# Optimization experiments

Measured on AMD Instinct MI355X. Metric: run time of the kernel, lower is better.

The kernel has to match this reference:

```python
import jax, jax.numpy as jnp
import numpy as np

B, T = 64, 512
OBS, DM, DS, NL = 115, 128, 8, 3
EMB, NA, H1 = 16, 19, 256


def _ln(x, g, b, eps=1e-5):
    m = jnp.mean(x, -1, keepdims=True)
    v = jnp.mean((x - m) ** 2, -1, keepdims=True)
    return (x - m) * jax.lax.rsqrt(v + eps) * g + b


def _s6(x, h, lng, lnb, w_ig, w_dt, b_dt, a_log, w_b, w_c, d_par, w_out):
    # x: [B,T,DM], h: [B,DM,DS]
    xn = _ln(x, lng, lnb)
    xp = xn @ w_ig.T                               # [B,T,2*DM]
    x_in, z = xp[..., :DM], xp[..., DM:]
    dt = jax.nn.softplus(x_in @ w_dt.T + b_dt)     # [B,T,DM]
    A = -jnp.exp(a_log)                            # [DM,DS]
    bt = x_in @ w_b.T                              # [B,T,DS]
    ct = x_in @ w_c.T                              # [B,T,DS]
    dA = jnp.exp(dt[..., None] * A)                # [B,T,DM,DS]
    upd = (dt * x_in)[..., None] * bt[:, :, None, :]  # [B,T,DM,DS]

    def step(hc, inp):
        dA_t, u_t, c_t = inp
        hn = dA_t * hc + u_t                       # [B,DM,DS]
        y = jnp.einsum('bds,bs->bd', hn, c_t)      # [B,DM]
        return hn, y

    h_f, ys = jax.lax.scan(
        step, h,
        (jnp.swapaxes(dA, 0, 1), jnp.swapaxes(upd, 0, 1), jnp.swapaxes(ct, 0, 1)))
    y = jnp.swapaxes(ys, 0, 1)                     # [B,T,DM]
    ssm = y * jax.nn.silu(z) + x_in * d_par
    return x + ssm @ w_out.T, h_f.reshape(h_f.shape[0], -1)


def _forward(prev_actions, obs, h0, enc_w1, enc_b1, enc_g1, enc_bb1, enc_w2, enc_b2,
             enc_g2, enc_bb2, emb, proj_w, proj_b, proj_g, proj_bb,
             m_ln_g, m_ln_b, m_w_ig, m_w_dt, m_b_dt, m_a_log, m_w_b, m_w_c, m_d, m_w_out,
             fn_g, fn_b, pol_w1, pol_b1, pol_g, pol_bb, pol_w2, pol_b2):
    # MLP encoder: Linear -> LN -> SiLU -> Linear -> LN (final norm)
    e = jax.nn.silu(_ln(obs @ enc_w1.T + enc_b1, enc_g1, enc_bb1))
    e = _ln(e @ enc_w2.T + enc_b2, enc_g2, enc_bb2)
    pa = emb[prev_actions]                         # [B,T,EMB]
    x = jnp.concatenate([e, pa], -1) @ proj_w.T + proj_b
    x = jax.nn.silu(_ln(x, proj_g, proj_bb))
    for i in range(NL):
        x, _ = _s6(x, h0[i].reshape(-1, DM, DS), m_ln_g[i], m_ln_b[i], m_w_ig[i],
                   m_w_dt[i], m_b_dt[i], m_a_log[i], m_w_b[i], m_w_c[i], m_d[i], m_w_out[i])
    x = _ln(x, fn_g, fn_b)
    p = jax.nn.silu(_ln(x @ pol_w1.T + pol_b1, pol_g, pol_bb))
    return p @ pol_w2.T + pol_b2                   # [B,T,NA] policy logits


def setup_inputs() -> dict:
    key = jax.random.key(0)
    ks = iter(jax.random.split(key, 64))
    def n(shape, s=0.05):
        return jax.random.normal(next(ks), shape, dtype=jnp.float32) * s
    return {
        'obs': jax.random.normal(next(ks), (B, T, OBS), dtype=jnp.float32),
        'h0': jnp.zeros((NL, B, DM * DS), jnp.float32),
        'enc_w1': n((H1, OBS)), 'enc_b1': jnp.zeros((H1,)),
        'enc_g1': jnp.ones((H1,)), 'enc_bb1': jnp.zeros((H1,)),
        'enc_w2': n((DM, H1)), 'enc_b2': jnp.zeros((DM,)),
        'enc_g2': jnp.ones((DM,)), 'enc_bb2': jnp.zeros((DM,)),
        'emb': n((NA + 1, EMB), 1.0),
        'proj_w': n((DM, DM + EMB)), 'proj_b': jnp.zeros((DM,)),
        'proj_g': jnp.ones((DM,)), 'proj_bb': jnp.zeros((DM,)),
        'm_ln_g': jnp.ones((NL, DM)), 'm_ln_b': jnp.zeros((NL, DM)),
        'm_w_ig': n((NL, 2 * DM, DM)), 'm_w_dt': n((NL, DM, DM)),
        'm_b_dt': jnp.zeros((NL, DM)),
        'm_a_log': jax.random.uniform(next(ks), (NL, DM, DS), minval=-3.0, maxval=-1.0, dtype=jnp.float32),
        'm_w_b': n((NL, DS, DM)), 'm_w_c': n((NL, DS, DM)),
        'm_d': jnp.ones((NL, DM)), 'm_w_out': n((NL, DM, DM)),
        'fn_g': jnp.ones((DM,)), 'fn_b': jnp.zeros((DM,)),
        'pol_w1': n((DM, DM)), 'pol_b1': jnp.zeros((DM,)),
        'pol_g': jnp.ones((DM,)), 'pol_bb': jnp.zeros((DM,)),
        'pol_w2': n((NA, DM)), 'pol_b2': jnp.zeros((NA,)),
        'prev_actions': jax.random.randint(next(ks), (B, T), 0, NA + 1),
    }


def reference(obs, h0, enc_w1, enc_b1, enc_g1, enc_bb1, enc_w2, enc_b2, enc_g2, enc_bb2,
              emb, proj_w, proj_b, proj_g, proj_bb, m_ln_g, m_ln_b, m_w_ig, m_w_dt,
              m_b_dt, m_a_log, m_w_b, m_w_c, m_d, m_w_out, fn_g, fn_b, pol_w1, pol_b1,
              pol_g, pol_bb, pol_w2, pol_b2, prev_actions):
    return _forward(prev_actions, obs, h0, enc_w1, enc_b1, enc_g1, enc_bb1, enc_w2,
                    enc_b2, enc_g2, enc_bb2, emb, proj_w, proj_b, proj_g, proj_bb,
                    m_ln_g, m_ln_b, m_w_ig, m_w_dt, m_b_dt, m_a_log, m_w_b, m_w_c,
                    m_d, m_w_out, fn_g, fn_b, pol_w1, pol_b1, pol_g, pol_bb, pol_w2, pol_b2)
```

## Files before the change

kernel.cpp:

```cpp
#include <hip/hip_runtime.h>
#include <math.h>

#define BB 64
#define TT 512
#define OBSD 115
#define DMD 128
#define DSD 8
#define NLD 3
#define EMBD 16
#define NAD 19
#define H1D 256
#define NTOK (BB*TT)
#define SSEG 16
#define TSEG (TT/SSEG)

typedef unsigned short ushort_t;
typedef __attribute__((ext_vector_type(8))) short short8;
typedef __attribute__((ext_vector_type(4))) float f32x4;

__device__ __forceinline__ float silu_f(float x){ return x / (1.f + __expf(-x)); }
__device__ __forceinline__ float softplus_f(float x){
  return fmaxf(x, 0.f) + log1pf(__expf(-fabsf(x)));
}
__device__ __forceinline__ ushort_t f2bf(float x){
  unsigned u = __float_as_uint(x);
  unsigned r = (u + 0x7fffu + ((u >> 16) & 1u)) >> 16;
  return (ushort_t)r;
}
__device__ __forceinline__ float b2f(ushort_t x){
  return __uint_as_float(((unsigned)x) << 16);
}
#define MFMA(a,b,c) __builtin_amdgcn_mfma_f32_16x16x32_bf16((a),(b),(c),0,0,0)
#define LOG2E 1.44269504f

template<int D, int SV>
__device__ __forceinline__ void ln32(const float* s_val, float* s_mr, int tid){
  const int t = tid >> 3, part = tid & 7;
  float s = 0.f, s2 = 0.f;
  #pragma unroll
  for (int j = part; j < D; j += 8){ float v = s_val[t*SV + j]; s += v; s2 = fmaf(v, v, s2); }
  s += __shfl_xor(s, 1, 64); s2 += __shfl_xor(s2, 1, 64);
  s += __shfl_xor(s, 2, 64); s2 += __shfl_xor(s2, 2, 64);
  s += __shfl_xor(s, 4, 64); s2 += __shfl_xor(s2, 4, 64);
  if (part == 0){
    float m = s * (1.f/(float)D);
    s_mr[t*2] = m;
    s_mr[t*2+1] = rsqrtf(s2 * (1.f/(float)D) - m*m + 1e-5f);
  }
}

struct PJob { const float* src; ushort_t* dst; int N; int K; int Kpad; int rowofs; int Nw; };
struct PJobs { PJob j[20]; };

__global__ __launch_bounds__(256) void k_prep(PJobs P){
  const int job = blockIdx.x >> 2;
  const int sub = blockIdx.x & 3;
  PJob pj = P.j[job];
  const int elems = pj.Nw * pj.Kpad;
  for (int idx = sub*256 + threadIdx.x; idx < elems; idx += 4*256){
    int n = idx / pj.Kpad;
    int k = idx - n*pj.Kpad;
    float v = (n < pj.N && k < pj.K) ? pj.src[(size_t)n*pj.K + k] : 0.f;
    pj.dst[(size_t)(pj.rowofs + n)*pj.Kpad + k] = f2bf(v);
  }
}

__global__ __launch_bounds__(256) void k_enc1(
    const float* __restrict__ obs, const ushort_t* __restrict__ w1b,
    const float* __restrict__ b1, const float* __restrict__ g1,
    const float* __restrict__ bb1, ushort_t* __restrict__ e1)
{
  __shared__ ushort_t s_a[32*136];
  __shared__ float s_val[32*264];
  __shared__ float s_mr[64];
  const int tok0 = blockIdx.x * 32;
  const int tid = threadIdx.x;
  const int lane = tid & 63, w = tid >> 6;
  const int q = lane >> 4, cn = lane & 15;
  const int m0 = (w & 1) * 16, nh = w >> 1;

  for (int e = tid; e < 32*16; e += 256){
    int t = e >> 4, kc = e & 15;
    const float* op = obs + (size_t)(tok0 + t)*OBSD;
    short8 v;
    #pragma unroll
    for (int j = 0; j < 8; j++){
      int k = kc*8 + j;
      v[j] = (short)f2bf(k < OBSD ? op[k] : 0.f);
    }
    *(short8*)&s_a[t*136 + kc*8] = v;
  }
  __syncthreads();

  short8 af[4];
  #pragma unroll
  for (int ks = 0; ks < 4; ks++)
    af[ks] = *(const short8*)&s_a[(m0 + cn)*136 + ks*32 + q*8];

  #pragma unroll
  for (int nt = 0; nt < 8; nt++){
    const int n0 = (nh*8 + nt) * 16;
    f32x4 acc = {0.f,0.f,0.f,0.f};
    #pragma unroll
    for (int ks = 0; ks < 4; ks++){
      short8 bf = *(const short8*)&w1b[(size_t)(n0 + cn)*128 + ks*32 + q*8];
      acc = MFMA(af[ks], bf, acc);
    }
    float bias = b1[n0 + cn];
    #pragma unroll
    for (int r = 0; r < 4; r++)
      s_val[(m0 + q*4 + r)*264 + n0 + cn] = acc[r] + bias;
  }
  __syncthreads();

  ln32<256,264>(s_val, s_mr, tid);
  __syncthreads();
  for (int e = tid; e < 32*256; e += 256){
    int t = e >> 8, c = e & 255;
    float v = (s_val[t*264 + c] - s_mr[t*2]) * s_mr[t*2+1] * g1[c] + bb1[c];
    e1[(size_t)(tok0 + t)*256 + c] = f2bf(silu_f(v));
  }
}

__global__ __launch_bounds__(256) void k_enc2p(
    const ushort_t* __restrict__ e1, const ushort_t* __restrict__ w2b,
    const float* __restrict__ b2, const float* __restrict__ g2,
    const float* __restrict__ bb2,
    const float* __restrict__ emb, const int* __restrict__ pact,
    const ushort_t* __restrict__ pwb, const float* __restrict__ pb,
    const float* __restrict__ pg, const float* __restrict__ pbb,
    float* __restrict__ X,
    const float* __restrict__ lng, const float* __restrict__ lnb,
    const ushort_t* __restrict__ wigb, const ushort_t* __restrict__ wdbcb,
    const float* __restrict__ bdt,
    ushort_t* __restrict__ XINb, ushort_t* __restrict__ Zb,
    ushort_t* __restrict__ DTb, ushort_t* __restrict__ BTu, ushort_t* __restrict__ CTu,
    const float* __restrict__ alog0,
    float* __restrict__ HLOC, float* __restrict__ PPR)
{
  __shared__ __align__(16) char sm[46336];
  float*    s_val = (float*)sm;
  ushort_t* s_a   = (ushort_t*)(sm + 17408);
  ushort_t* s_xin = (ushort_t*)(sm + 28160);
  ushort_t* s_dt  = (ushort_t*)(sm + 36864);
  ushort_t* s_btc = (ushort_t*)(sm + 45568);
  float*    s_mr  = (float*)(sm + 46080);

  const int tok0 = blockIdx.x * 32;
  const int bidx = blockIdx.x >> 4;
  const int ch   = blockIdx.x & 15;
  const int tid = threadIdx.x;
  const int lane = tid & 63, w = tid >> 6;
  const int q = lane >> 4, cn = lane & 15;
  const int m0 = (w & 1) * 16, nh = w >> 1;

  for (int e = tid; e < 32*32; e += 256){
    int t = e >> 5, k = e & 31;
    float v = 0.f;
    if (k < EMBD){ int a = pact[tok0 + t]; v = emb[(size_t)a*EMBD + k]; }
    s_a[t*168 + 128 + k] = f2bf(v);
  }
  {
    short8 af[8];
    #pragma unroll
    for (int ks = 0; ks < 8; ks++)
      af[ks] = *(const short8*)&e1[(size_t)(tok0 + m0 + cn)*256 + ks*32 + q*8];
    #pragma unroll
    for (int nt = 0; nt < 4; nt++){
      const int n0 = (nh*4 + nt) * 16;
      f32x4 acc = {0.f,0.f,0.f,0.f};
      #pragma unroll
      for (int ks = 0; ks < 8; ks++){
        short8 bf = *(const short8*)&w2b[(size_t)(n0 + cn)*256 + ks*32 + q*8];
        acc = MFMA(af[ks], bf, acc);
      }
      float bias = b2[n0 + cn];
      #pragma unroll
      for (int r = 0; r < 4; r++)
        s_val[(m0 + q*4 + r)*136 + n0 + cn] = acc[r] + bias;
    }
  }
  __syncthreads();

  ln32<128,136>(s_val, s_mr, tid);
  __syncthreads();
  for (int e = tid; e < 32*128; e += 256){
    int t = e >> 7, c = e & 127;
    float v = (s_val[t*136 + c] - s_mr[t*2]) * s_mr[t*2+1] * g2[c] + bb2[c];
    s_a[t*168 + c] = f2bf(v);
  }
  __syncthreads();

  {
    short8 af2[5];
    #pragma unroll
    for (int ks = 0; ks < 5; ks++)
      af2[ks] = *(const short8*)&s_a[(m0 + cn)*168 + ks*32 + q*8];
    #pragma unroll
    for (int nt = 0; nt < 4; nt++){
      const int n0 = (nh*4 + nt) * 16;
      f32x4 acc = {0.f,0.f,0.f,0.f};
      #pragma unroll
      for (int ks = 0; ks < 5; ks++){
        short8 bf = *(const short8*)&pwb[(size_t)(n0 + cn)*160 + ks*32 + q*8];
        acc = MFMA(af2[ks], bf, acc);
      }
      float bias = pb[n0 + cn];
      #pragma unroll
      for (int r = 0; r < 4; r++)
        s_val[(m0 + q*4 + r)*136 + n0 + cn] = acc[r] + bias;
    }
  }
  __syncthreads();

  ln32<128,136>(s_val, s_mr, tid);
  __syncthreads();
  for (int e = tid; e < 32*128; e += 256){
    int t = e >> 7, c = e & 127;
    float v = (s_val[t*136 + c] - s_mr[t*2]) * s_mr[t*2+1] * pg[c] + pbb[c];
    v = silu_f(v);
    X[(size_t)tok0*128 + e] = v;
    s_val[t*136 + c] = v;
  }
  __syncthreads();

  ln32<128,136>(s_val, s_mr, tid);
  __syncthreads();
  for (int e = tid; e < 32*128; e += 256){
    int t = e >> 7, c = e & 127;
    float v = (s_val[t*136 + c] - s_mr[t*2]) * s_mr[t*2+1] * lng[c] + lnb[c];
    s_a[t*168 + c] = f2bf(v);
  }
  __syncthreads();

  {
    short8 af[4];
    #pragma unroll
    for (int ks = 0; ks < 4; ks++)
      af[ks] = *(const short8*)&s_a[(m0 + cn)*168 + ks*32 + q*8];
    #pragma unroll
    for (int nt = 0; nt < 8; nt++){
      const int n0 = (nh*8 + nt) * 16;
      f32x4 acc = {0.f,0.f,0.f,0.f};
      #pragma unroll
      for (int ks = 0; ks < 4; ks++){
        short8 bf = *(const short8*)&wigb[(size_t)(n0 + cn)*128 + ks*32 + q*8];
        acc = MFMA(af[ks], bf, acc);
      }
      if (n0 < 128){
        #pragma unroll
        for (int r = 0; r < 4; r++){
          int tr = m0 + q*4 + r;
          ushort_t bb = f2bf(acc[r]);
          XINb[(size_t)(tok0 + tr)*128 + n0 + cn] = bb;
          s_xin[tr*136 + n0 + cn] = bb;
        }
      } else {
        #pragma unroll
        for (int r = 0; r < 4; r++){
          int tr = m0 + q*4 + r;
          Zb[(size_t)(tok0 + tr)*128 + (n0 - 128) + cn] = f2bf(acc[r]);
        }
      }
    }
  }
  __syncthreads();

  {
    short8 af2[4];
    #pragma unroll
    for (int ks = 0; ks < 4; ks++)
      af2[ks] = *(const short8*)&s_xin[(m0 + cn)*136 + ks*32 + q*8];
    for (int nt = nh; nt < 9; nt += 2){
      const int n0 = nt * 16;
      f32x4 acc = {0.f,0.f,0.f,0.f};
      #pragma unroll
      for (int ks = 0; ks < 4; ks++){
        short8 bf = *(const short8*)&wdbcb[(size_t)(n0 + cn)*128 + ks*32 + q*8];
        acc = MFMA(af2[ks], bf, acc);
      }
      const int col = n0 + cn;
      if (col < 128){
        float bd = bdt[col];
        #pragma unroll
        for (int r = 0; r < 4; r++){
          int tr = m0 + q*4 + r;
          ushort_t dv = f2bf(softplus_f(acc[r] + bd));
          DTb[(size_t)(tok0 + tr)*128 + col] = dv;
          s_dt[tr*136 + col] = dv;
        }
      } else if (col < 136){
        #pragma unroll
        for (int r = 0; r < 4; r++){
          int tr = m0 + q*4 + r;
          ushort_t bb = f2bf(acc[r]);
          BTu[(size_t)(tok0 + tr)*8 + (col - 128)] = bb;
          s_btc[tr*8 + (col - 128)] = bb;
        }
      } else {
        #pragma unroll
        for (int r = 0; r < 4; r++)
          CTu[(size_t)(tok0 + m0 + q*4 + r)*8 + (col - 136)] = f2bf(acc[r]);
      }
    }
  }
  __syncthreads();

  {
    const int d = tid & 127, sh = tid >> 7;
    float A2c[4], hh[4], pp[4];
    #pragma unroll
    for (int j = 0; j < 4; j++){
      A2c[j] = -__expf(alog0[d*8 + sh*4 + j]) * LOG2E;
      hh[j] = 0.f; pp[j] = 1.f;
    }
    for (int t = 0; t < 32; t++){
      float dt = b2f(s_dt[t*136 + d]);
      float wv = dt * b2f(s_xin[t*136 + d]);
      #pragma unroll
      for (int j = 0; j < 4; j++){
        float dA = exp2f(dt * A2c[j]);
        hh[j] = fmaf(dA, hh[j], wv * b2f(s_btc[t*8 + sh*4 + j]));
        pp[j] *= dA;
      }
    }
    const size_t o = ((size_t)bidx*16 + ch)*1024 + d*8 + sh*4;
    #pragma unroll
    for (int j = 0; j < 4; j++){ HLOC[o+j] = hh[j]; PPR[o+j] = pp[j]; }
  }
}

__global__ __launch_bounds__(256) void k_carry(
    const float* __restrict__ h0g,
    const float* __restrict__ HL, const float* __restrict__ PP,
    float* __restrict__ HST)
{
  const int b = blockIdx.x;
  const int qd = threadIdx.x;
  float4 H = *(const float4*)(h0g + (size_t)b*1024 + qd*4);
  for (int sg = 0; sg < SSEG; sg++){
    *(float4*)(HST + ((size_t)b*SSEG + sg)*1024 + qd*4) = H;
    float4 hl = *(const float4*)(HL + ((size_t)b*SSEG + sg)*1024 + qd*4);
    float4 pp = *(const float4*)(PP + ((size_t)b*SSEG + sg)*1024 + qd*4);
    H.x = fmaf(pp.x, H.x, hl.x); H.y = fmaf(pp.y, H.y, hl.y);
    H.z = fmaf(pp.z, H.z, hl.z); H.w = fmaf(pp.w, H.w, hl.w);
  }
}

#define SMS 34560

__device__ __forceinline__ void phaseB_post(
    const ushort_t* DTb, const ushort_t* XINb, const ushort_t* Zb,
    const ushort_t* BTu, const ushort_t* CTu,
    const float* __restrict__ alog, const float* __restrict__ HST,
    const float* __restrict__ dpar, const ushort_t* __restrict__ woutb,
    float* __restrict__ X, char* sm, int b, int sg)
{
  ushort_t* s_dtS = (ushort_t*)sm;
  ushort_t* s_xiS = (ushort_t*)(sm + 8192);
  ushort_t* s_zS  = (ushort_t*)(sm + 16384);
  ushort_t* s_a   = (ushort_t*)(sm + 24576);
  float*    s_x   = (float*)sm;
  ushort_t* s_bt  = (ushort_t*)(sm + 33280);
  ushort_t* s_ct  = (ushort_t*)(sm + 33792);
  float*    s_mr  = (float*)(sm + 34304);

  const int tid = threadIdx.x;
  const int d = tid;
  const int w = tid >> 6, lane = tid & 63, q = lane >> 4, cn = lane & 15;
  const size_t segtok = (size_t)b*TT + sg*TSEG;

  {
    const uint4* gdt = (const uint4*)(DTb + segtok*128);
    const uint4* gxi = (const uint4*)(XINb + segtok*128);
    const uint4* gz  = (const uint4*)(Zb + segtok*128);
    #pragma unroll
    for (int i = 0; i < 4; i++){
      ((uint4*)s_dtS)[tid + i*128] = gdt[tid + i*128];
      ((uint4*)s_xiS)[tid + i*128] = gxi[tid + i*128];
      ((uint4*)s_zS )[tid + i*128] = gz [tid + i*128];
    }
    ((unsigned*)s_bt)[tid] = ((const unsigned*)(BTu + segtok*8))[tid];
    ((unsigned*)s_ct)[tid] = ((const unsigned*)(CTu + segtok*8))[tid];
  }
  float A2[8], h[8];
  #pragma unroll
  for (int s = 0; s < 8; s++){
    A2[s] = -__expf(alog[d*8 + s]) * LOG2E;
    h[s] = HST[((size_t)b*SSEG + sg)*1024 + d*8 + s];
  }
  const float dp = dpar[d];
  __syncthreads();

  #pragma unroll 4
  for (int t = 0; t < 32; t++){
    float dt = b2f(s_dtS[t*128 + d]);
    float xi = b2f(s_xiS[t*128 + d]);
    float wv = dt * xi;
    float y = 0.f;
    #pragma unroll
    for (int s = 0; s < 8; s++){
      float dA = exp2f(dt * A2[s]);
      h[s] = fmaf(dA, h[s], wv * b2f(s_bt[t*8 + s]));
      y = fmaf(h[s], b2f(s_ct[t*8 + s]), y);
    }
    float ssm = y * silu_f(b2f(s_zS[t*128 + d])) + xi * dp;
    s_a[t*136 + d] = f2bf(ssm);
  }
  __syncthreads();

  {
    short8 af[2][4];
    #pragma unroll
    for (int mt = 0; mt < 2; mt++)
      #pragma unroll
      for (int ks = 0; ks < 4; ks++)
        af[mt][ks] = *(const short8*)&s_a[(mt*16 + cn)*136 + ks*32 + q*8];
    for (int nt = w; nt < 8; nt += 2){
      const int n0 = nt * 16;
      short8 bf[4];
      #pragma unroll
      for (int ks = 0; ks < 4; ks++)
        bf[ks] = *(const short8*)&woutb[(size_t)(n0+cn)*128 + ks*32 + q*8];
      #pragma unroll
      for (int mt = 0; mt < 2; mt++){
        f32x4 acc = {0.f,0.f,0.f,0.f};
        #pragma unroll
        for (int ks = 0; ks < 4; ks++) acc = MFMA(af[mt][ks], bf[ks], acc);
        #pragma unroll
        for (int r = 0; r < 4; r++){
          const int tr = mt*16 + q*4 + r;
          const size_t g = (segtok + tr)*128 + n0 + cn;
          float xn = X[g] + acc[r];
          X[g] = xn;
          s_x[tr*130 + n0 + cn] = xn;
        }
      }
    }
  }
  __syncthreads();

  {
    const int t = tid >> 2, qtr = tid & 3;
    float s = 0.f, s2 = 0.f;
    const float* row = s_x + t*130 + qtr*32;
    for (int j = 0; j < 32; j++){ float v = row[j]; s += v; s2 = fmaf(v, v, s2); }
    s  += __shfl_xor(s, 1, 64);  s2 += __shfl_xor(s2, 1, 64);
    s  += __shfl_xor(s, 2, 64);  s2 += __shfl_xor(s2, 2, 64);
    float m = s * (1.f/128.f);
    float var = s2 * (1.f/128.f) - m*m;
    if (qtr == 0){ s_mr[t*2] = m; s_mr[t*2+1] = rsqrtf(var + 1e-5f); }
  }
  __syncthreads();
}

__global__ __launch_bounds__(128) void k_scan2p(
    ushort_t* DTb, ushort_t* XINb, ushort_t* Zb,
    ushort_t* BTu, ushort_t* CTu,
    const float* __restrict__ alog, const float* __restrict__ HST,
    const float* __restrict__ dpar, const ushort_t* __restrict__ woutb,
    float* __restrict__ X,
    const float* __restrict__ lng, const float* __restrict__ lnb,
    const ushort_t* __restrict__ wigb, const ushort_t* __restrict__ wdbcb,
    const float* __restrict__ bdt,
    const float* __restrict__ alogn,
    float* __restrict__ HLOC, float* __restrict__ PPR)
{
  __shared__ __align__(16) char sm[SMS];
  ushort_t* s_a  = (ushort_t*)(sm + 24576);
  float*    s_x  = (float*)sm;
  ushort_t* s_xin= (ushort_t*)sm;
  ushort_t* s_bt = (ushort_t*)(sm + 33280);
  float*    s_mr = (float*)(sm + 34304);

  const int b = blockIdx.x >> 4, sg = blockIdx.x & 15;
  const int tid = threadIdx.x;
  const int w = tid >> 6, lane = tid & 63, q = lane >> 4, cn = lane & 15;
  const size_t segtok = (size_t)b*TT + sg*TSEG;

  phaseB_post(DTb, XINb, Zb, BTu, CTu, alog, HST, dpar, woutb, X, sm, b, sg);

  {
    float g = lng[tid], c0 = lnb[tid];
    for (int t = 0; t < 32; t++){
      float v = (s_x[t*130 + tid] - s_mr[t*2]) * s_mr[t*2+1] * g + c0;
      s_a[t*136 + tid] = f2bf(v);
    }
  }
  __syncthreads();

  {
    short8 af[2][4];
    #pragma unroll
    for (int mt = 0; mt < 2; mt++)
      #pragma unroll
      for (int ks = 0; ks < 4; ks++)
        af[mt][ks] = *(const short8*)&s_a[(mt*16 + cn)*136 + ks*32 + q*8];
    for (int nt = w; nt < 16; nt += 2){
      const int n0 = nt * 16;
      short8 bf[4];
      #pragma unroll
      for (int ks = 0; ks < 4; ks++)
        bf[ks] = *(const short8*)&wigb[(size_t)(n0+cn)*128 + ks*32 + q*8];
      #pragma unroll
      for (int mt = 0; mt < 2; mt++){
        f32x4 acc = {0.f,0.f,0.f,0.f};
        #pragma unroll
        for (int ks = 0; ks < 4; ks++) acc = MFMA(af[mt][ks], bf[ks], acc);
        if (n0 < 128){
          #pragma unroll
          for (int r = 0; r < 4; r++){
            const int tr = mt*16 + q*4 + r;
            ushort_t bb = f2bf(acc[r]);
            XINb[(segtok + tr)*128 + n0 + cn] = bb;
            s_xin[tr*136 + n0 + cn] = bb;
          }
        } else {
          #pragma unroll
          for (int r = 0; r < 4; r++){
            const int tr = mt*16 + q*4 + r;
            Zb[(segtok + tr)*128 + (n0-128) + cn] = f2bf(acc[r]);
          }
        }
      }
    }
  }
  __syncthreads();

  {
    short8 af[2][4];
    #pragma unroll
    for (int mt = 0; mt < 2; mt++)
      #pragma unroll
      for (int ks = 0; ks < 4; ks++)
        af[mt][ks] = *(const short8*)&s_xin[(mt*16 + cn)*136 + ks*32 + q*8];
    for (int nt = w; nt < 9; nt += 2){
      const int n0 = nt * 16;
      short8 bf[4];
      #pragma unroll
      for (int ks = 0; ks < 4; ks++)
        bf[ks] = *(const short8*)&wdbcb[(size_t)(n0+cn)*128 + ks*32 + q*8];
      const int col = n0 + cn;
      #pragma unroll
      for (int mt = 0; mt < 2; mt++){
        f32x4 acc = {0.f,0.f,0.f,0.f};
        #pragma unroll
        for (int ks = 0; ks < 4; ks++) acc = MFMA(af[mt][ks], bf[ks], acc);
        if (col < 128){
          float bd = bdt[col];
          #pragma unroll
          for (int r = 0; r < 4; r++){
            const int tr = mt*16 + q*4 + r;
            ushort_t dv = f2bf(softplus_f(acc[r] + bd));
            DTb[(segtok + tr)*128 + col] = dv;
            s_a[tr*136 + col] = dv;
          }
        } else if (col < 136){
          #pragma unroll
          for (int r = 0; r < 4; r++){
            const int tr = mt*16 + q*4 + r;
            ushort_t bb = f2bf(acc[r]);
            BTu[(segtok + tr)*8 + (col-128)] = bb;
            s_bt[tr*8 + (col-128)] = bb;
          }
        } else {
          #pragma unroll
          for (int r = 0; r < 4; r++)
            CTu[(segtok + mt*16 + q*4 + r)*8 + (col-136)] = f2bf(acc[r]);
        }
      }
    }
  }
  __syncthreads();

  {
    float A2n[8], hh[8], pp[8];
    #pragma unroll
    for (int s = 0; s < 8; s++){
      A2n[s] = -__expf(alogn[tid*8 + s]) * LOG2E;
      hh[s] = 0.f; pp[s] = 1.f;
    }
    for (int t = 0; t < 32; t++){
      float dt = b2f(s_a[t*136 + tid]);
      float wv = dt * b2f(s_xin[t*136 + tid]);
      #pragma unroll
      for (int s = 0; s < 8; s++){
        float dA = exp2f(dt * A2n[s]);
        hh[s] = fmaf(dA, hh[s], wv * b2f(s_bt[t*8 + s]));
        pp[s] *= dA;
      }
    }
    const size_t o = ((size_t)b*SSEG + sg)*1024 + tid*8;
    #pragma unroll
    for (int s = 0; s < 8; s++){ HLOC[o+s] = hh[s]; PPR[o+s] = pp[s]; }
  }
}

__global__ __launch_bounds__(128) void k_scan2h(
    const ushort_t* DTb, const ushort_t* XINb, const ushort_t* Zb,
    const ushort_t* BTu, const ushort_t* CTu,
    const float* __restrict__ alog, const float* __restrict__ HST,
    const float* __restrict__ dpar, const ushort_t* __restrict__ woutb,
    float* __restrict__ X,
    const float* __restrict__ fng, const float* __restrict__ fnb,
    const ushort_t* __restrict__ pw1b, const float* __restrict__ pb1,
    const float* __restrict__ pg, const float* __restrict__ pbb,
    const ushort_t* __restrict__ pw2b, const float* __restrict__ pb2,
    float* __restrict__ out)
{
  __shared__ __align__(16) char sm[SMS];
  ushort_t* s_a  = (ushort_t*)(sm + 24576);
  float*    s_x  = (float*)sm;
  float*    s_mr = (float*)(sm + 34304);

  const int b = blockIdx.x >> 4, sg = blockIdx.x & 15;
  const int tid = threadIdx.x;
  const int w = tid >> 6, lane = tid & 63, q = lane >> 4, cn = lane & 15;
  const size_t segtok = (size_t)b*TT + sg*TSEG;

  phaseB_post((ushort_t*)DTb, (ushort_t*)XINb, (ushort_t*)Zb,
              (ushort_t*)BTu, (ushort_t*)CTu, alog, HST, dpar, woutb, X, sm, b, sg);

  {
    float g = fng[tid], c0 = fnb[tid];
    for (int t = 0; t < 32; t++){
      float v = (s_x[t*130 + tid] - s_mr[t*2]) * s_mr[t*2+1] * g + c0;
      s_a[t*136 + tid] = f2bf(v);
    }
  }
  __syncthreads();

  {
    short8 af[2][4];
    #pragma unroll
    for (int mt = 0; mt < 2; mt++)
      #pragma unroll
      for (int ks = 0; ks < 4; ks++)
        af[mt][ks] = *(const short8*)&s_a[(mt*16 + cn)*136 + ks*32 + q*8];
    for (int nt = w; nt < 8; nt += 2){
      const int n0 = nt * 16;
      short8 bf[4];
      #pragma unroll
      for (int ks = 0; ks < 4; ks++)
        bf[ks] = *(const short8*)&pw1b[(size_t)(n0+cn)*128 + ks*32 + q*8];
      float bias = pb1[n0 + cn];
      #pragma unroll
      for (int mt = 0; mt < 2; mt++){
        f32x4 acc = {0.f,0.f,0.f,0.f};
        #pragma unroll
        for (int ks = 0; ks < 4; ks++) acc = MFMA(af[mt][ks], bf[ks], acc);
        #pragma unroll
        for (int r = 0; r < 4; r++)
          s_x[(mt*16 + q*4 + r)*130 + n0 + cn] = acc[r] + bias;
      }
    }
  }
  __syncthreads();

  {
    const int t = tid >> 2, qtr = tid & 3;
    float s = 0.f, s2 = 0.f;
    const float* row = s_x + t*130 + qtr*32;
    for (int j = 0; j < 32; j++){ float v = row[j]; s += v; s2 = fmaf(v, v, s2); }
    s  += __shfl_xor(s, 1, 64);  s2 += __shfl_xor(s2, 1, 64);
    s  += __shfl_xor(s, 2, 64);  s2 += __shfl_xor(s2, 2, 64);
    float m = s * (1.f/128.f);
    float var = s2 * (1.f/128.f) - m*m;
    if (qtr == 0){ s_mr[t*2] = m; s_mr[t*2+1] = rsqrtf(var + 1e-5f); }
  }
  __syncthreads();
  {
    float g = pg[tid], c0 = pbb[tid];
    for (int t = 0; t < 32; t++){
      float v = (s_x[t*130 + tid] - s_mr[t*2]) * s_mr[t*2+1] * g + c0;
      s_a[t*136 + tid] = f2bf(silu_f(v));
    }
  }
  __syncthreads();

  {
    short8 af[2][4];
    #pragma unroll
    for (int mt = 0; mt < 2; mt++)
      #pragma unroll
      for (int ks = 0; ks < 4; ks++)
        af[mt][ks] = *(const short8*)&s_a[(mt*16 + cn)*136 + ks*32 + q*8];
    const int n0 = w * 16;
    short8 bf[4];
    #pragma unroll
    for (int ks = 0; ks < 4; ks++)
      bf[ks] = *(const short8*)&pw2b[(size_t)(n0+cn)*128 + ks*32 + q*8];
    const int col = n0 + cn;
    #pragma unroll
    for (int mt = 0; mt < 2; mt++){
      f32x4 acc = {0.f,0.f,0.f,0.f};
      #pragma unroll
      for (int ks = 0; ks < 4; ks++) acc = MFMA(af[mt][ks], bf[ks], acc);
      if (col < NAD){
        float bias = pb2[col];
        #pragma unroll
        for (int r = 0; r < 4; r++)
          out[(segtok + mt*16 + q*4 + r)*NAD + col] = acc[r] + bias;
      }
    }
  }
}

extern "C" void kernel_launch(void* const* d_in, const int* in_sizes, int n_in,
                              void* d_out, int out_size, void* d_ws, size_t ws_size,
                              hipStream_t stream) {
  const float* obs    = (const float*)d_in[0];
  const float* h0     = (const float*)d_in[1];
  const float* enc_w1 = (const float*)d_in[2];
  const float* enc_b1 = (const float*)d_in[3];
  const float* enc_g1 = (const float*)d_in[4];
  const float* enc_bb1= (const float*)d_in[5];
  const float* enc_w2 = (const float*)d_in[6];
  const float* enc_b2 = (const float*)d_in[7];
  const float* enc_g2 = (const float*)d_in[8];
  const float* enc_bb2= (const float*)d_in[9];
  const float* emb    = (const float*)d_in[10];
  const float* proj_w = (const float*)d_in[11];
  const float* proj_b = (const float*)d_in[12];
  const float* proj_g = (const float*)d_in[13];
  const float* proj_bb= (const float*)d_in[14];
  const float* m_ln_g = (const float*)d_in[15];
  const float* m_ln_b = (const float*)d_in[16];
  const float* m_w_ig = (const float*)d_in[17];
  const float* m_w_dt = (const float*)d_in[18];
  const float* m_b_dt = (const float*)d_in[19];
  const float* m_a_log= (const float*)d_in[20];
  const float* m_w_b  = (const float*)d_in[21];
  const float* m_w_c  = (const float*)d_in[22];
  const float* m_d    = (const float*)d_in[23];
  const float* m_w_out= (const float*)d_in[24];
  const float* fn_g   = (const float*)d_in[25];
  const float* fn_b   = (const float*)d_in[26];
  const float* pol_w1 = (const float*)d_in[27];
  const float* pol_b1 = (const float*)d_in[28];
  const float* pol_g  = (const float*)d_in[29];
  const float* pol_bb = (const float*)d_in[30];
  const float* pol_w2 = (const float*)d_in[31];
  const float* pol_b2 = (const float*)d_in[32];
  const int*   pact   = (const int*)d_in[33];

  float* ws  = (float*)d_ws;
  float* X    = ws;
  float* HLOC = X + (size_t)NTOK*128;
  float* PPR  = HLOC + (size_t)BB*16*1024;
  float* HST  = PPR  + (size_t)BB*16*1024;
  ushort_t* E1   = (ushort_t*)(HST + (size_t)BB*16*1024);
  ushort_t* XINb = E1   + (size_t)NTOK*256;
  ushort_t* Zb   = XINb + (size_t)NTOK*128;
  ushort_t* DTb  = Zb   + (size_t)NTOK*128;
  ushort_t* BTu  = DTb  + (size_t)NTOK*128;
  ushort_t* CTu  = BTu  + (size_t)NTOK*8;

  ushort_t* W1B   = CTu   + (size_t)NTOK*8;
  ushort_t* W2B   = W1B   + 256*128;
  ushort_t* PWB   = W2B   + 128*256;
  ushort_t* WIGB  = PWB   + 128*160;
  ushort_t* WDBCB = WIGB  + 3*256*128;
  ushort_t* WOUTB = WDBCB + 3*144*128;
  ushort_t* PW1B  = WOUTB + 3*128*128;
  ushort_t* PW2B  = PW1B  + 128*128;

  PJobs P;
  int nj = 0;
  auto add = [&](const float* src, ushort_t* dst, int N, int K, int Kpad, int rowofs, int Nw){
    P.j[nj].src = src; P.j[nj].dst = dst; P.j[nj].N = N; P.j[nj].K = K;
    P.j[nj].Kpad = Kpad; P.j[nj].rowofs = rowofs; P.j[nj].Nw = Nw; nj++;
  };
  add(enc_w1, W1B, 256, 115, 128, 0, 256);
  add(enc_w2, W2B, 128, 256, 256, 0, 128);
  add(proj_w, PWB, 128, 144, 160, 0, 128);
  for (int l = 0; l < NLD; l++)
    add(m_w_ig + (size_t)l*256*128, WIGB + (size_t)l*256*128, 256, 128, 128, 0, 256);
  for (int l = 0; l < NLD; l++){
    add(m_w_dt + (size_t)l*128*128, WDBCB + (size_t)l*144*128, 128, 128, 128, 0,   128);
    add(m_w_b  + (size_t)l*8*128,   WDBCB + (size_t)l*144*128,   8, 128, 128, 128,   8);
    add(m_w_c  + (size_t)l*8*128,   WDBCB + (size_t)l*144*128,   8, 128, 128, 136,   8);
  }
  for (int l = 0; l < NLD; l++)
    add(m_w_out + (size_t)l*128*128, WOUTB + (size_t)l*128*128, 128, 128, 128, 0, 128);
  add(pol_w1, PW1B, 128, 128, 128, 0, 128);
  add(pol_w2, PW2B,  19, 128, 128, 0,  32);

  k_prep<<<20*4, 256, 0, stream>>>(P);
  k_enc1<<<NTOK/32, 256, 0, stream>>>(obs, W1B, enc_b1, enc_g1, enc_bb1, E1);
  k_enc2p<<<NTOK/32, 256, 0, stream>>>(E1, W2B, enc_b2, enc_g2, enc_bb2,
      emb, pact, PWB, proj_b, proj_g, proj_bb, X,
      m_ln_g, m_ln_b, WIGB, WDBCB, m_b_dt,
      XINb, Zb, DTb, BTu, CTu,
      m_a_log, HLOC, PPR);

  k_carry<<<BB, 256, 0, stream>>>(h0, HLOC, PPR, HST);
  k_scan2p<<<BB*SSEG, 128, 0, stream>>>(DTb, XINb, Zb, BTu, CTu,
      m_a_log, HST, m_d, WOUTB, X,
      m_ln_g + 128, m_ln_b + 128,
      WIGB + (size_t)256*128, WDBCB + (size_t)144*128, m_b_dt + 128,
      m_a_log + 1024, HLOC, PPR);
  k_carry<<<BB, 256, 0, stream>>>(h0 + (size_t)BB*1024, HLOC, PPR, HST);
  k_scan2p<<<BB*SSEG, 128, 0, stream>>>(DTb, XINb, Zb, BTu, CTu,
      m_a_log + 1024, HST, m_d + 128, WOUTB + (size_t)128*128, X,
      m_ln_g + 256, m_ln_b + 256,
      WIGB + (size_t)2*256*128, WDBCB + (size_t)2*144*128, m_b_dt + 256,
      m_a_log + 2048, HLOC, PPR);
  k_carry<<<BB, 256, 0, stream>>>(h0 + (size_t)2*BB*1024, HLOC, PPR, HST);
  k_scan2h<<<BB*SSEG, 128, 0, stream>>>(DTb, XINb, Zb, BTu, CTu,
      m_a_log + 2048, HST, m_d + 256, WOUTB + (size_t)2*128*128, X,
      fn_g, fn_b, PW1B, pol_b1, pol_g, pol_bb, PW2B, pol_b2,
      (float*)d_out);
}
```

Measured before the change: 406.0 us.

## Fold segment carry scan into scan kernels and shrink shared memory footprints

Removes the three separate k_carry launches. Each scan block now rebuilds its own starting state by walking the per-segment local states and decay products of earlier segments. Because blocks read the previous layer's HL/PP while writing new ones, the buffers are double-buffered (A/B ping-pong). Shared memory in k_enc1 and k_enc2p is also aliased, with an extra barrier, to lower LDS usage and raise occupancy. In exchange, later segments repeat up to 15 redundant carry steps and extra global reads.

```diff
diff --git a/kernel.cpp b/kernel.cpp
--- a/kernel.cpp
+++ b/kernel.cpp
@@ -70,9 +70,10 @@
     const float* __restrict__ b1, const float* __restrict__ g1,
     const float* __restrict__ bb1, ushort_t* __restrict__ e1)
 {
-  __shared__ ushort_t s_a[32*136];
-  __shared__ float s_val[32*264];
-  __shared__ float s_mr[64];
+  __shared__ __align__(16) char sm[34048];
+  float*    s_val = (float*)sm;
+  ushort_t* s_a   = (ushort_t*)sm;
+  float*    s_mr  = (float*)(sm + 33792);
   const int tok0 = blockIdx.x * 32;
   const int tid = threadIdx.x;
   const int lane = tid & 63, w = tid >> 6;
@@ -96,6 +97,7 @@
   #pragma unroll
   for (int ks = 0; ks < 4; ks++)
     af[ks] = *(const short8*)&s_a[(m0 + cn)*136 + ks*32 + q*8];
+  __syncthreads();
 
   #pragma unroll
   for (int nt = 0; nt < 8; nt++){
@@ -138,13 +140,13 @@
     const float* __restrict__ alog0,
     float* __restrict__ HLOC, float* __restrict__ PPR)
 {
-  __shared__ __align__(16) char sm[46336];
+  __shared__ __align__(16) char sm[28928];
   float*    s_val = (float*)sm;
+  ushort_t* s_xin = (ushort_t*)sm;
+  ushort_t* s_dt  = (ushort_t*)(sm + 8704);
   ushort_t* s_a   = (ushort_t*)(sm + 17408);
-  ushort_t* s_xin = (ushort_t*)(sm + 28160);
-  ushort_t* s_dt  = (ushort_t*)(sm + 36864);
-  ushort_t* s_btc = (ushort_t*)(sm + 45568);
-  float*    s_mr  = (float*)(sm + 46080);
+  ushort_t* s_btc = (ushort_t*)(sm + 28160);
+  float*    s_mr  = (float*)(sm + 28672);
 
   const int tok0 = blockIdx.x * 32;
   const int bidx = blockIdx.x >> 4;
@@ -330,29 +332,13 @@
   }
 }
 
-__global__ __launch_bounds__(256) void k_carry(
-    const float* __restrict__ h0g,
-    const float* __restrict__ HL, const float* __restrict__ PP,
-    float* __restrict__ HST)
-{
-  const int b = blockIdx.x;
-  const int qd = threadIdx.x;
-  float4 H = *(const float4*)(h0g + (size_t)b*1024 + qd*4);
-  for (int sg = 0; sg < SSEG; sg++){
-    *(float4*)(HST + ((size_t)b*SSEG + sg)*1024 + qd*4) = H;
-    float4 hl = *(const float4*)(HL + ((size_t)b*SSEG + sg)*1024 + qd*4);
-    float4 pp = *(const float4*)(PP + ((size_t)b*SSEG + sg)*1024 + qd*4);
-    H.x = fmaf(pp.x, H.x, hl.x); H.y = fmaf(pp.y, H.y, hl.y);
-    H.z = fmaf(pp.z, H.z, hl.z); H.w = fmaf(pp.w, H.w, hl.w);
-  }
-}
-
 #define SMS 34560
 
 __device__ __forceinline__ void phaseB_post(
     const ushort_t* DTb, const ushort_t* XINb, const ushort_t* Zb,
     const ushort_t* BTu, const ushort_t* CTu,
-    const float* __restrict__ alog, const float* __restrict__ HST,
+    const float* __restrict__ alog, const float* __restrict__ h0g,
+    const float* __restrict__ HLi, const float* __restrict__ PPi,
     const float* __restrict__ dpar, const ushort_t* __restrict__ woutb,
     float* __restrict__ X, char* sm, int b, int sg)
 {
@@ -387,7 +373,18 @@
   #pragma unroll
   for (int s = 0; s < 8; s++){
     A2[s] = -__expf(alog[d*8 + s]) * LOG2E;
-    h[s] = HST[((size_t)b*SSEG + sg)*1024 + d*8 + s];
+    h[s] = h0g[(size_t)b*1024 + d*8 + s];
+  }
+  for (int ch = 0; ch < sg; ch++){
+    const size_t o = ((size_t)b*SSEG + ch)*1024 + d*8;
+    float4 hl0 = *(const float4*)(HLi + o);
+    float4 hl1 = *(const float4*)(HLi + o + 4);
+    float4 pp0 = *(const float4*)(PPi + o);
+    float4 pp1 = *(const float4*)(PPi + o + 4);
+    h[0]=fmaf(pp0.x,h[0],hl0.x); h[1]=fmaf(pp0.y,h[1],hl0.y);
+    h[2]=fmaf(pp0.z,h[2],hl0.z); h[3]=fmaf(pp0.w,h[3],hl0.w);
+    h[4]=fmaf(pp1.x,h[4],hl1.x); h[5]=fmaf(pp1.y,h[5],hl1.y);
+    h[6]=fmaf(pp1.z,h[6],hl1.z); h[7]=fmaf(pp1.w,h[7],hl1.w);
   }
   const float dp = dpar[d];
   __syncthreads();
@@ -457,14 +454,15 @@
 __global__ __launch_bounds__(128) void k_scan2p(
     ushort_t* DTb, ushort_t* XINb, ushort_t* Zb,
     ushort_t* BTu, ushort_t* CTu,
-    const float* __restrict__ alog, const float* __restrict__ HST,
+    const float* __restrict__ alog, const float* __restrict__ h0g,
+    const float* __restrict__ HLi, const float* __restrict__ PPi,
     const float* __restrict__ dpar, const ushort_t* __restrict__ woutb,
     float* __restrict__ X,
     const float* __restrict__ lng, const float* __restrict__ lnb,
     const ushort_t* __restrict__ wigb, const ushort_t* __restrict__ wdbcb,
     const float* __restrict__ bdt,
     const float* __restrict__ alogn,
-    float* __restrict__ HLOC, float* __restrict__ PPR)
+    float* __restrict__ HLo, float* __restrict__ PPo)
 {
   __shared__ __align__(16) char sm[SMS];
   ushort_t* s_a  = (ushort_t*)(sm + 24576);
@@ -478,7 +476,7 @@
   const int w = tid >> 6, lane = tid & 63, q = lane >> 4, cn = lane & 15;
   const size_t segtok = (size_t)b*TT + sg*TSEG;
 
-  phaseB_post(DTb, XINb, Zb, BTu, CTu, alog, HST, dpar, woutb, X, sm, b, sg);
+  phaseB_post(DTb, XINb, Zb, BTu, CTu, alog, h0g, HLi, PPi, dpar, woutb, X, sm, b, sg);
 
   {
     float g = lng[tid], c0 = lnb[tid];
@@ -592,14 +590,15 @@
     }
     const size_t o = ((size_t)b*SSEG + sg)*1024 + tid*8;
     #pragma unroll
-    for (int s = 0; s < 8; s++){ HLOC[o+s] = hh[s]; PPR[o+s] = pp[s]; }
+    for (int s = 0; s < 8; s++){ HLo[o+s] = hh[s]; PPo[o+s] = pp[s]; }
   }
 }
 
 __global__ __launch_bounds__(128) void k_scan2h(
     const ushort_t* DTb, const ushort_t* XINb, const ushort_t* Zb,
     const ushort_t* BTu, const ushort_t* CTu,
-    const float* __restrict__ alog, const float* __restrict__ HST,
+    const float* __restrict__ alog, const float* __restrict__ h0g,
+    const float* __restrict__ HLi, const float* __restrict__ PPi,
     const float* __restrict__ dpar, const ushort_t* __restrict__ woutb,
     float* __restrict__ X,
     const float* __restrict__ fng, const float* __restrict__ fnb,
@@ -619,7 +618,8 @@
   const size_t segtok = (size_t)b*TT + sg*TSEG;
 
   phaseB_post((ushort_t*)DTb, (ushort_t*)XINb, (ushort_t*)Zb,
-              (ushort_t*)BTu, (ushort_t*)CTu, alog, HST, dpar, woutb, X, sm, b, sg);
+              (ushort_t*)BTu, (ushort_t*)CTu, alog, h0g, HLi, PPi,
+              dpar, woutb, X, sm, b, sg);
 
   {
     float g = fng[tid], c0 = fnb[tid];
@@ -746,10 +746,11 @@
 
   float* ws  = (float*)d_ws;
   float* X    = ws;
-  float* HLOC = X + (size_t)NTOK*128;
-  float* PPR  = HLOC + (size_t)BB*16*1024;
-  float* HST  = PPR  + (size_t)BB*16*1024;
-  ushort_t* E1   = (ushort_t*)(HST + (size_t)BB*16*1024);
+  float* HLA  = X + (size_t)NTOK*128;
+  float* PPA  = HLA + (size_t)BB*16*1024;
+  float* HLB  = PPA + (size_t)BB*16*1024;
+  float* PPB  = HLB + (size_t)BB*16*1024;
+  ushort_t* E1   = (ushort_t*)(PPB + (size_t)BB*16*1024);
   ushort_t* XINb = E1   + (size_t)NTOK*256;
   ushort_t* Zb   = XINb + (size_t)NTOK*128;
   ushort_t* DTb  = Zb   + (size_t)NTOK*128;
@@ -792,23 +793,22 @@
       emb, pact, PWB, proj_b, proj_g, proj_bb, X,
       m_ln_g, m_ln_b, WIGB, WDBCB, m_b_dt,
       XINb, Zb, DTb, BTu, CTu,
-      m_a_log, HLOC, PPR);
-
-  k_carry<<<BB, 256, 0, stream>>>(h0, HLOC, PPR, HST);
+      m_a_log, HLA, PPA);
+
   k_scan2p<<<BB*SSEG, 128, 0, stream>>>(DTb, XINb, Zb, BTu, CTu,
-      m_a_log, HST, m_d, WOUTB, X,
+      m_a_log, h0, HLA, PPA, m_d, WOUTB, X,
       m_ln_g + 128, m_ln_b + 128,
       WIGB + (size_t)256*128, WDBCB + (size_t)144*128, m_b_dt + 128,
-      m_a_log + 1024, HLOC, PPR);
-  k_carry<<<BB, 256, 0, stream>>>(h0 + (size_t)BB*1024, HLOC, PPR, HST);
+      m_a_log + 1024, HLB, PPB);
   k_scan2p<<<BB*SSEG, 128, 0, stream>>>(DTb, XINb, Zb, BTu, CTu,
-      m_a_log + 1024, HST, m_d + 128, WOUTB + (size_t)128*128, X,
+      m_a_log + 1024, h0 + (size_t)BB*1024, HLB, PPB, m_d + 128,
+      WOUTB + (size_t)128*128, X,
       m_ln_g + 256, m_ln_b + 256,
       WIGB + (size_t)2*256*128, WDBCB + (size_t)2*144*128, m_b_dt + 256,
-      m_a_log + 2048, HLOC, PPR);
-  k_carry<<<BB, 256, 0, stream>>>(h0 + (size_t)2*BB*1024, HLOC, PPR, HST);
+      m_a_log + 2048, HLA, PPA);
   k_scan2h<<<BB*SSEG, 128, 0, stream>>>(DTb, XINb, Zb, BTu, CTu,
-      m_a_log + 2048, HST, m_d + 256, WOUTB + (size_t)2*128*128, X,
+      m_a_log + 2048, h0 + (size_t)2*BB*1024, HLA, PPA, m_d + 256,
+      WOUTB + (size_t)2*128*128, X,
       fn_g, fn_b, PW1B, pol_b1, pol_g, pol_bb, PW2B, pol_b2,
       (float*)d_out);
 }
```

Measured after the change: 405.9 us. No clear change (-0.0%).
